# Performance work log

Hardware: AMD Instinct MI355X
Metric: run time of the kernel (lower is better)

Reference implementation:

```python
import jax, jax.numpy as jnp
import numpy as np

B, S, R, H = 32, 512, 49, 768


def setup_inputs() -> dict:
    key = jax.random.key(0)
    ks = jax.random.split(key, 32)
    rn = lambda i, shape, s=1.0: jax.random.normal(ks[i], shape, dtype=jnp.float32) * s
    W = 0.05  # weight init scale to keep tanh/softmax in a sane range
    return {
        'text_features': rn(0, (B, S, H)),
        'img_features': rn(1, (B, R, H)),
        't1_w': rn(2, (H, H), W), 't1_b': rn(3, (H,), W),
        'i1_w': rn(4, (H, H), W),
        'a1_w': rn(5, (2 * H,), W), 'a1_b': rn(6, (), W),
        't2_w': rn(7, (H, H), W),
        'i2_w': rn(8, (H, H), W), 'i2_b': rn(9, (H,), W),
        'a2_w': rn(10, (2 * H,), W), 'a2_b': rn(11, (), W),
        'gt_w': rn(12, (H, H), W), 'gt_b': rn(13, (H,), W),
        'gi_w': rn(14, (H, H), W), 'gi_b': rn(15, (H,), W),
        'gg_w': rn(16, (2 * H, 1), W), 'gg_b': rn(17, (1,), W),
        'ft_w': rn(18, (H, H), W),
        'fm_w': rn(19, (H, H), W), 'fm_b': rn(20, (H,), W),
        'fg_w': rn(21, (2 * H, 1), W), 'fg_b': rn(22, (1,), W),
        'fr_w': rn(23, (H, H), W), 'fr_b': rn(24, (H,), W),
    }


def reference(text_features, img_features, t1_w, t1_b, i1_w, a1_w, a1_b,
              t2_w, i2_w, i2_b, a2_w, a2_b, gt_w, gt_b, gi_w, gi_b,
              gg_w, gg_b, ft_w, fm_w, fm_b, fg_w, fg_b, fr_w, fr_b):
    H = text_features.shape[-1]
    # --- CoAttention, stage 1 (text attends over image regions) ---
    # tanh(concat) is elementwise and att_linear_1 is rank-1, so split the score:
    # score[b,s,r] = tanh(t1(x_s)) . a1[:H] + tanh(i1(y_r)) . a1[H:] + b
    t_sc = jnp.tanh(text_features @ t1_w + t1_b) @ a1_w[:H]          # (B,S)
    i_sc = jnp.tanh(img_features @ i1_w) @ a1_w[H:]                  # (B,R)
    visual_att = jax.nn.softmax(t_sc[:, :, None] + i_sc[:, None, :] + a1_b, axis=-1)  # (B,S,R)
    att_img = jnp.einsum('bsr,brh->bsh', visual_att, img_features)   # (B,S,H)
    # --- CoAttention, stage 2 (attended-image queries attend over text) ---
    # concat order is [img, text] -> a2[:H] pairs with img part
    q_sc = jnp.tanh(att_img @ i2_w + i2_b) @ a2_w[:H]                # (B,S)
    k_sc = jnp.tanh(text_features @ t2_w) @ a2_w[H:]                 # (B,S)
    textual_att = jax.nn.softmax(q_sc[:, :, None] + k_sc[:, None, :] + a2_b, axis=-1)  # (B,S,S)
    att_text = jnp.einsum('bij,bjh->bih', textual_att, text_features)  # (B,S,H)
    # --- GMF gated fusion ---
    new_img = jnp.tanh(att_img @ gi_w + gi_b)
    new_txt = jnp.tanh(att_text @ gt_w + gt_b)
    gate = jax.nn.sigmoid(jnp.concatenate([new_img, new_txt], axis=-1) @ gg_w + gg_b)  # (B,S,1)
    multimodal = gate * new_img + (1.0 - gate) * new_txt
    # --- filtration gate ---
    concat_feat = jnp.concatenate([text_features @ ft_w, multimodal @ fm_w + fm_b], axis=-1)
    fgate = jax.nn.sigmoid(concat_feat @ fg_w + fg_b)                # (B,S,1)
    return fgate * jnp.tanh(multimodal @ fr_w + fr_b)
```

## Files before the change

### kernel.cpp

```cpp
#include <hip/hip_runtime.h>
#include <hip/hip_bf16.h>
#include <math.h>

constexpr int BD = 32;
constexpr int SD = 512;
constexpr int RD = 49;
constexpr int HD = 768;
constexpr int NB = HD / 64;
constexpr int NP = NB * 2;
constexpr int MT = BD * SD;
constexpr int MI = BD * RD;

typedef __bf16 bf16;
typedef __bf16 bf16x4 __attribute__((ext_vector_type(4)));
typedef __bf16 bf16x8 __attribute__((ext_vector_type(8)));
typedef float f32x4 __attribute__((ext_vector_type(4)));

__global__ __launch_bounds__(256) void prep_text(
    const float* __restrict__ text, const float* __restrict__ v_f,
    bf16* __restrict__ text_bf, float* __restrict__ s_txt)
{
    const int row = blockIdx.x * 4 + (threadIdx.x >> 6);
    const int lane = threadIdx.x & 63;
    const float* tr = text + (size_t)row * HD;
    bf16* tb = text_bf + (size_t)row * HD;
    float acc = 0.f;
    #pragma unroll
    for (int c = 0; c < 3; ++c) {
        const int o = c * 256 + lane * 4;
        const f32x4 x = *(const f32x4*)(tr + o);
        const f32x4 v = *(const f32x4*)(v_f + o);
        bf16x4 b; b[0] = (bf16)x[0]; b[1] = (bf16)x[1]; b[2] = (bf16)x[2]; b[3] = (bf16)x[3];
        *(bf16x4*)(tb + o) = b;
        acc += x[0] * v[0] + x[1] * v[1] + x[2] * v[2] + x[3] * v[3];
    }
    for (int off = 32; off; off >>= 1) acc += __shfl_xor(acc, off);
    if (lane == 0) s_txt[row] = acc;
}

__global__ __launch_bounds__(256) void conv_img(const float* __restrict__ src,
                                                bf16* __restrict__ dst, int n8) {
    const int i = blockIdx.x * 256 + threadIdx.x;
    if (i >= n8) return;
    const size_t o = (size_t)i * 8;
    const f32x4 x0 = *(const f32x4*)(src + o);
    const f32x4 x1 = *(const f32x4*)(src + o + 4);
    bf16x8 b;
    b[0]=(bf16)x0[0]; b[1]=(bf16)x0[1]; b[2]=(bf16)x0[2]; b[3]=(bf16)x0[3];
    b[4]=(bf16)x1[0]; b[5]=(bf16)x1[1]; b[6]=(bf16)x1[2]; b[7]=(bf16)x1[3];
    *(bf16x8*)(dst + o) = b;
}

__global__ __launch_bounds__(256) void transpose_w(
    const float* __restrict__ w0, const float* __restrict__ w1,
    bf16* __restrict__ o0, bf16* __restrict__ o1)
{
    __shared__ float tile[64][65];
    const float* W = blockIdx.z ? w1 : w0;
    bf16* Wt = blockIdx.z ? o1 : o0;
    const int k0 = blockIdx.x * 64, n0 = blockIdx.y * 64;
    const int t = threadIdx.x;
    const int rb = t >> 6, c = t & 63;
    #pragma unroll
    for (int i = 0; i < 16; ++i) {
        const int r = rb + i * 4;
        tile[r][c] = W[(size_t)(k0 + r) * HD + n0 + c];
    }
    __syncthreads();
    #pragma unroll
    for (int i = 0; i < 16; ++i) {
        const int r = rb + i * 4;
        Wt[(size_t)(n0 + r) * HD + k0 + c] = (bf16)tile[c][r];
    }
}

__global__ __launch_bounds__(256) void gemm_bt(
    const bf16* __restrict__ A, const bf16* __restrict__ Wt,
    const float* __restrict__ vec, float* __restrict__ part, int M)
{
    __shared__ __align__(16) bf16 As[64][40];
    __shared__ __align__(16) bf16 Bs[64][40];

    const int t = threadIdx.x;
    const int m0 = blockIdx.x * 64;
    const int n0 = blockIdx.y * 64;
    const int w = t >> 6, lane = t & 63;
    const int quad = lane >> 4, l16 = lane & 15;
    const int wm = (w >> 1) * 32, wn = (w & 1) * 32;

    const int r = t >> 2, c8 = (t & 3) * 8;
    const int gm = m0 + r;
    const bf16* Ap = A + (size_t)gm * HD + c8;
    const bf16* Bp = Wt + (size_t)(n0 + r) * HD + c8;

    f32x4 acc[2][2] = {};

    for (int kk = 0; kk < HD; kk += 32) {
        bf16x8 av = {};
        if (gm < M) av = *(const bf16x8*)(Ap + kk);
        const bf16x8 bv = *(const bf16x8*)(Bp + kk);

        __syncthreads();
        *(bf16x8*)(&As[r][c8]) = av;
        *(bf16x8*)(&Bs[r][c8]) = bv;
        __syncthreads();

        const bf16x8 a0 = *(const bf16x8*)(&As[wm + l16][quad * 8]);
        const bf16x8 a1 = *(const bf16x8*)(&As[wm + 16 + l16][quad * 8]);
        const bf16x8 b0 = *(const bf16x8*)(&Bs[wn + l16][quad * 8]);
        const bf16x8 b1 = *(const bf16x8*)(&Bs[wn + 16 + l16][quad * 8]);
        acc[0][0] = __builtin_amdgcn_mfma_f32_16x16x32_bf16(a0, b0, acc[0][0], 0, 0, 0);
        acc[0][1] = __builtin_amdgcn_mfma_f32_16x16x32_bf16(a0, b1, acc[0][1], 0, 0, 0);
        acc[1][0] = __builtin_amdgcn_mfma_f32_16x16x32_bf16(a1, b0, acc[1][0], 0, 0, 0);
        acc[1][1] = __builtin_amdgcn_mfma_f32_16x16x32_bf16(a1, b1, acc[1][1], 0, 0, 0);
    }

    #pragma unroll
    for (int ti = 0; ti < 2; ++ti)
      #pragma unroll
      for (int reg = 0; reg < 4; ++reg) {
          float p = 0.f;
          #pragma unroll
          for (int tj = 0; tj < 2; ++tj) {
              const int gn = n0 + wn + tj * 16 + l16;
              p += tanhf(acc[ti][tj][reg]) * vec[gn];
          }
          p += __shfl_xor(p, 1);
          p += __shfl_xor(p, 2);
          p += __shfl_xor(p, 4);
          p += __shfl_xor(p, 8);
          const int gm2 = m0 + wm + ti * 16 + quad * 4 + reg;
          if (l16 == 0) part[(size_t)gm2 * NP + blockIdx.y * 2 + (w & 1)] = p;
      }
}

__global__ __launch_bounds__(256) void reduce_nb(const float* __restrict__ part,
                                                 float* __restrict__ score, int M) {
    const int m = blockIdx.x * 256 + threadIdx.x;
    if (m < M) {
        float s = 0.f;
        #pragma unroll
        for (int j = 0; j < NP; ++j) s += part[(size_t)m * NP + j];
        score[m] = s;
    }
}

__global__ __launch_bounds__(64) void softmax_p1(const float* sc, float* p1) {
    const int b = blockIdx.x, l = threadIdx.x;
    float x = (l < RD) ? sc[b * RD + l] : -1e30f;
    float m = x;
    for (int off = 32; off; off >>= 1) m = fmaxf(m, __shfl_xor(m, off));
    float e = (l < RD) ? expf(x - m) : 0.f;
    float s = e;
    for (int off = 32; off; off >>= 1) s += __shfl_xor(s, off);
    if (l < RD) p1[b * RD + l] = e / s;
}

__global__ __launch_bounds__(256) void softmax_p2(const float* sc, float* p2) {
    const int b = blockIdx.x, t = threadIdx.x;
    __shared__ float red[4];
    const float x0 = sc[b * SD + t], x1 = sc[b * SD + 256 + t];
    float m = fmaxf(x0, x1);
    for (int off = 32; off; off >>= 1) m = fmaxf(m, __shfl_xor(m, off));
    if ((t & 63) == 0) red[t >> 6] = m;
    __syncthreads();
    m = fmaxf(fmaxf(red[0], red[1]), fmaxf(red[2], red[3]));
    const float e0 = expf(x0 - m), e1 = expf(x1 - m);
    float s = e0 + e1;
    for (int off = 32; off; off >>= 1) s += __shfl_xor(s, off);
    __syncthreads();
    if ((t & 63) == 0) red[t >> 6] = s;
    __syncthreads();
    s = red[0] + red[1] + red[2] + red[3];
    p2[b * SD + t] = e0 / s;
    p2[b * SD + 256 + t] = e1 / s;
}

__global__ __launch_bounds__(256) void wsum_rows(const float* __restrict__ P,
                                                 const float* __restrict__ X,
                                                 float* __restrict__ Y, int J) {
    const int b = blockIdx.x;
    const int h = blockIdx.y * 256 + threadIdx.x;
    __shared__ float Ps[SD];
    for (int j = threadIdx.x; j < J; j += 256) Ps[j] = P[b * J + j];
    __syncthreads();
    float acc = 0.f;
    const float* Xb = X + (size_t)b * J * HD + h;
    for (int j = 0; j < J; ++j) acc += Ps[j] * Xb[(size_t)j * HD];
    Y[b * HD + h] = acc;
}

__global__ __launch_bounds__(256) void wsum_part(const float* __restrict__ P,
                                                 const bf16* __restrict__ X,
                                                 float* __restrict__ part) {
    const int b = blockIdx.x;
    const int h = blockIdx.y * 256 + threadIdx.x;
    const int q = blockIdx.z;
    __shared__ float Ps[128];
    if (threadIdx.x < 128) Ps[threadIdx.x] = P[b * SD + q * 128 + threadIdx.x];
    __syncthreads();
    float acc = 0.f;
    const bf16* Xb = X + (size_t)b * SD * HD + (size_t)(q * 128) * HD + h;
    #pragma unroll 8
    for (int j = 0; j < 128; ++j) acc += Ps[j] * (float)Xb[(size_t)j * HD];
    part[((size_t)(b * 4 + q)) * HD + h] = acc;
}

__global__ __launch_bounds__(256) void wsum_reduce(const float* __restrict__ part,
                                                   float* __restrict__ Y) {
    const int m = blockIdx.x * 256 + threadIdx.x;
    const int b = m / HD, h = m % HD;
    float s = 0.f;
    #pragma unroll
    for (int q = 0; q < 4; ++q) s += part[((size_t)(b * 4 + q)) * HD + h];
    Y[m] = s;
}

__global__ __launch_bounds__(256) void ni_nt_kernel(
    const float* __restrict__ aimg, const float* __restrict__ atxt,
    const float* __restrict__ gi_w, const float* __restrict__ gi_b,
    const float* __restrict__ gt_w, const float* __restrict__ gt_b,
    float* __restrict__ ni, float* __restrict__ nt)
{
    const int b = blockIdx.x, n0 = blockIdx.y * 64, which = blockIdx.z;
    const float* X = which ? atxt : aimg;
    const float* W = which ? gt_w : gi_w;
    const float* bias = which ? gt_b : gi_b;
    float* Y = which ? nt : ni;

    __shared__ float Xs[HD];
    __shared__ float partial[4][64];
    const int t = threadIdx.x;
    for (int h = t; h < HD; h += 256) Xs[h] = X[b * HD + h];
    __syncthreads();
    const int n = n0 + (t & 63), kq = t >> 6;
    float acc = 0.f;
    const float* Wp = W + (size_t)(kq * 192) * HD + n;
    #pragma unroll 8
    for (int h = 0; h < 192; ++h) acc += Xs[kq * 192 + h] * Wp[(size_t)h * HD];
    partial[kq][t & 63] = acc;
    __syncthreads();
    if (t < 64) {
        const float s = partial[0][t] + partial[1][t] + partial[2][t] + partial[3][t];
        Y[b * HD + n0 + t] = tanhf(s + bias[n0 + t]);
    }
}

__global__ __launch_bounds__(256) void gate_mix(
    const float* __restrict__ ni, const float* __restrict__ nt,
    const float* __restrict__ gg_w, const float* __restrict__ gg_b,
    const float* __restrict__ v_m, const float* __restrict__ c_m,
    const float* __restrict__ fg_b,
    float* __restrict__ mm, float* __restrict__ s_mm)
{
    const int b = blockIdx.x, t = threadIdx.x;
    __shared__ float red[4];
    __shared__ float gsh;
    float acc = 0.f;
    for (int n = t; n < HD; n += 256)
        acc += ni[b * HD + n] * gg_w[n] + nt[b * HD + n] * gg_w[HD + n];
    for (int off = 32; off; off >>= 1) acc += __shfl_xor(acc, off);
    if ((t & 63) == 0) red[t >> 6] = acc;
    __syncthreads();
    if (t == 0) gsh = 1.f / (1.f + expf(-(red[0] + red[1] + red[2] + red[3] + gg_b[0])));
    __syncthreads();
    const float g = gsh;
    float a2 = 0.f;
    for (int n = t; n < HD; n += 256) {
        const float m = g * ni[b * HD + n] + (1.f - g) * nt[b * HD + n];
        mm[b * HD + n] = m;
        a2 += m * v_m[n];
    }
    for (int off = 32; off; off >>= 1) a2 += __shfl_xor(a2, off);
    __syncthreads();
    if ((t & 63) == 0) red[t >> 6] = a2;
    __syncthreads();
    if (t == 0) s_mm[b] = red[0] + red[1] + red[2] + red[3] + *c_m + fg_b[0];
}

__global__ __launch_bounds__(256) void T_kernel(
    const float* __restrict__ mm, const float* __restrict__ fr_w,
    const float* __restrict__ fr_b, float* __restrict__ T)
{
    const int b = blockIdx.x, n0 = blockIdx.y * 64;
    __shared__ float Xs[HD];
    __shared__ float partial[4][64];
    const int t = threadIdx.x;
    for (int h = t; h < HD; h += 256) Xs[h] = mm[b * HD + h];
    __syncthreads();
    const int n = n0 + (t & 63), kq = t >> 6;
    float acc = 0.f;
    const float* Wp = fr_w + (size_t)(kq * 192) * HD + n;
    #pragma unroll 8
    for (int h = 0; h < 192; ++h) acc += Xs[kq * 192 + h] * Wp[(size_t)h * HD];
    partial[kq][t & 63] = acc;
    __syncthreads();
    if (t < 64) {
        const float s = partial[0][t] + partial[1][t] + partial[2][t] + partial[3][t];
        T[b * HD + n0 + t] = tanhf(s + fr_b[n0 + t]);
    }
}

__global__ __launch_bounds__(256) void vf_vm_kernel(const float* __restrict__ ft_w,
                                                    const float* __restrict__ fm_w,
                                                    const float* __restrict__ fm_b,
                                                    const float* __restrict__ fg_w,
                                                    float* __restrict__ v_f,
                                                    float* __restrict__ v_m,
                                                    float* __restrict__ c_m) {
    const int idx = blockIdx.x * 4 + (threadIdx.x >> 6);
    const int lane = threadIdx.x & 63;
    const float* row; const float* vecp; float* outp;
    if (idx < HD)            { row = ft_w + (size_t)idx * HD;        vecp = fg_w;      outp = v_f + idx; }
    else if (idx < 2 * HD)   { row = fm_w + (size_t)(idx - HD) * HD; vecp = fg_w + HD; outp = v_m + (idx - HD); }
    else if (idx == 2 * HD)  { row = fm_b;                           vecp = fg_w + HD; outp = c_m; }
    else return;
    float acc = 0.f;
    #pragma unroll
    for (int i = 0; i < HD / 64; ++i) acc += row[lane + 64 * i] * vecp[lane + 64 * i];
    for (int off = 32; off; off >>= 1) acc += __shfl_xor(acc, off);
    if (lane == 0) *outp = acc;
}

__global__ __launch_bounds__(256) void out_kernel(const float* __restrict__ s_txt,
                                                  const float* __restrict__ s_mm,
                                                  const float* __restrict__ T,
                                                  float* __restrict__ out) {
    const size_t idx = ((size_t)blockIdx.x * 256 + threadIdx.x) * 4;
    const int h = (int)(idx % HD);
    const int bs = (int)(idx / HD);
    const int b = bs >> 9;
    float f = s_txt[bs] + s_mm[b];
    f = 1.f / (1.f + expf(-f));
    const float* Tp = T + b * HD + h;
    f32x4 o;
    o[0] = f * Tp[0]; o[1] = f * Tp[1]; o[2] = f * Tp[2]; o[3] = f * Tp[3];
    *(f32x4*)(out + idx) = o;
}

extern "C" void kernel_launch(void* const* d_in, const int* in_sizes, int n_in,
                              void* d_out, int out_size, void* d_ws, size_t ws_size,
                              hipStream_t stream) {
    const float* text = (const float*)d_in[0];
    const float* img  = (const float*)d_in[1];
    const float* i1_w = (const float*)d_in[4];
    const float* a1_w = (const float*)d_in[5];
    const float* t2_w = (const float*)d_in[7];
    const float* a2_w = (const float*)d_in[10];
    const float* gt_w = (const float*)d_in[12];
    const float* gt_b = (const float*)d_in[13];
    const float* gi_w = (const float*)d_in[14];
    const float* gi_b = (const float*)d_in[15];
    const float* gg_w = (const float*)d_in[16];
    const float* gg_b = (const float*)d_in[17];
    const float* ft_w = (const float*)d_in[18];
    const float* fm_w = (const float*)d_in[19];
    const float* fm_b = (const float*)d_in[20];
    const float* fg_w = (const float*)d_in[21];
    const float* fg_b = (const float*)d_in[22];
    const float* fr_w = (const float*)d_in[23];
    const float* fr_b = (const float*)d_in[24];
    float* out = (float*)d_out;

    float* sc_ = out;
    float* i_part  = sc_;
    float* k_part  = sc_ + 38400;
    float* i_sc    = sc_ + 431616;
    float* k_sc    = sc_ + 433216;
    float* aimg    = sc_ + 449600;
    float* atxt    = sc_ + 474176;
    float* v_f     = sc_ + 498752;
    float* v_m     = sc_ + 499520;
    float* c_m     = sc_ + 500288;
    float* ws_part = sc_ + 500352;
    float* ni      = sc_ + 598656;
    float* nt      = sc_ + 623232;
    float* mm      = sc_ + 647808;
    bf16* text_bf  = (bf16*)(sc_ + 672384);
    bf16* img_bf   = (bf16*)(sc_ + 6963840);
    bf16* wt_t     = (bf16*)(sc_ + 7565952);
    bf16* wt_i     = (bf16*)(sc_ + 7860864);

    float* ws    = (float*)d_ws;
    float* s_txt = ws;
    float* s_mm  = ws + 16384;
    float* T     = ws + 16448;

    vf_vm_kernel<<<dim3((2 * HD + 1 + 3) / 4), dim3(256), 0, stream>>>(
        ft_w, fm_w, fm_b, fg_w, v_f, v_m, c_m);
    prep_text<<<dim3(MT / 4), dim3(256), 0, stream>>>(text, v_f, text_bf, s_txt);
    conv_img<<<dim3((BD * RD * HD / 8 + 255) / 256), dim3(256), 0, stream>>>(
        img, img_bf, BD * RD * HD / 8);
    transpose_w<<<dim3(12, 12, 2), dim3(256), 0, stream>>>(t2_w, i1_w, wt_t, wt_i);
    gemm_bt<<<dim3((MI + 63) / 64, NB), dim3(256), 0, stream>>>(
        img_bf, wt_i, a1_w + HD, i_part, MI);
    gemm_bt<<<dim3(MT / 64, NB), dim3(256), 0, stream>>>(
        text_bf, wt_t, a2_w + HD, k_part, MT);
    reduce_nb<<<dim3(7), dim3(256), 0, stream>>>(i_part, i_sc, MI);
    reduce_nb<<<dim3(MT / 256), dim3(256), 0, stream>>>(k_part, k_sc, MT);
    softmax_p1<<<dim3(BD), dim3(64), 0, stream>>>(i_sc, i_sc);
    softmax_p2<<<dim3(BD), dim3(256), 0, stream>>>(k_sc, k_sc);
    wsum_rows<<<dim3(BD, HD / 256), dim3(256), 0, stream>>>(i_sc, img, aimg, RD);
    wsum_part<<<dim3(BD, HD / 256, 4), dim3(256), 0, stream>>>(k_sc, text_bf, ws_part);
    wsum_reduce<<<dim3(BD * HD / 256), dim3(256), 0, stream>>>(ws_part, atxt);
    ni_nt_kernel<<<dim3(BD, HD / 64, 2), dim3(256), 0, stream>>>(
        aimg, atxt, gi_w, gi_b, gt_w, gt_b, ni, nt);
    gate_mix<<<dim3(BD), dim3(256), 0, stream>>>(
        ni, nt, gg_w, gg_b, v_m, c_m, fg_b, mm, s_mm);
    T_kernel<<<dim3(BD, HD / 64), dim3(256), 0, stream>>>(mm, fr_w, fr_b, T);
    out_kernel<<<dim3((MT * HD / 4) / 256), dim3(256), 0, stream>>>(s_txt, s_mm, T, out);
}
```

Measured before the change: 293.9 us.

## Retile score GEMM with direct-to-LDS loads and merge small kernels

Replaces the two 64x64 score GEMMs with one combined launch. It uses 128x128 tiles, a 4x4 MFMA fragment grid per wave and global_load_lds to copy tiles straight into shared memory, and swaps tanhf for an exp-based fast tanh in the epilogue. It also merges weight prep, image conversion and transpose, the two reductions, the two softmaxes and the two weighted sums into single launches. The text weighted-sum reduction moves into the gating kernel. The goal is more data reuse in the dominant GEMM and fewer kernel launches, at the cost of unpadded LDS tiles that may bank-conflict and padded image rows that read past the image buffer into neighbouring scratch.

```diff
diff --git a/kernel.cpp b/kernel.cpp
--- a/kernel.cpp
+++ b/kernel.cpp
@@ -6,15 +6,25 @@
 constexpr int SD = 512;
 constexpr int RD = 49;
 constexpr int HD = 768;
-constexpr int NB = HD / 64;
-constexpr int NP = NB * 2;
 constexpr int MT = BD * SD;
 constexpr int MI = BD * RD;
+constexpr int NP = 12;
+constexpr int MBT = MT / 128;
+constexpr int MBI = 13;
 
 typedef __bf16 bf16;
 typedef __bf16 bf16x4 __attribute__((ext_vector_type(4)));
 typedef __bf16 bf16x8 __attribute__((ext_vector_type(8)));
 typedef float f32x4 __attribute__((ext_vector_type(4)));
+
+#define GLOAD_LDS16(g, l) __builtin_amdgcn_global_load_lds( \
+    (__attribute__((address_space(1))) void*)(g),           \
+    (__attribute__((address_space(3))) void*)(l), 16, 0, 0)
+
+__device__ __forceinline__ float fast_tanh(float x) {
+    const float e = __expf(2.f * x);
+    return 1.f - 2.f / (e + 1.f);
+}
 
 __global__ __launch_bounds__(256) void prep_text(
     const float* __restrict__ text, const float* __restrict__ v_f,
@@ -38,192 +48,234 @@
     if (lane == 0) s_txt[row] = acc;
 }
 
-__global__ __launch_bounds__(256) void conv_img(const float* __restrict__ src,
-                                                bf16* __restrict__ dst, int n8) {
-    const int i = blockIdx.x * 256 + threadIdx.x;
-    if (i >= n8) return;
-    const size_t o = (size_t)i * 8;
-    const f32x4 x0 = *(const f32x4*)(src + o);
-    const f32x4 x1 = *(const f32x4*)(src + o + 4);
-    bf16x8 b;
-    b[0]=(bf16)x0[0]; b[1]=(bf16)x0[1]; b[2]=(bf16)x0[2]; b[3]=(bf16)x0[3];
-    b[4]=(bf16)x1[0]; b[5]=(bf16)x1[1]; b[6]=(bf16)x1[2]; b[7]=(bf16)x1[3];
-    *(bf16x8*)(dst + o) = b;
-}
-
-__global__ __launch_bounds__(256) void transpose_w(
-    const float* __restrict__ w0, const float* __restrict__ w1,
-    bf16* __restrict__ o0, bf16* __restrict__ o1)
+__global__ __launch_bounds__(256) void prep_misc(
+    const float* __restrict__ ft_w, const float* __restrict__ fm_w,
+    const float* __restrict__ fm_b, const float* __restrict__ fg_w,
+    float* __restrict__ v_f, float* __restrict__ v_m, float* __restrict__ c_m,
+    const float* __restrict__ img, bf16* __restrict__ img_bf,
+    const float* __restrict__ t2_w, const float* __restrict__ i1_w,
+    bf16* __restrict__ wt_t, bf16* __restrict__ wt_i)
 {
     __shared__ float tile[64][65];
-    const float* W = blockIdx.z ? w1 : w0;
-    bf16* Wt = blockIdx.z ? o1 : o0;
-    const int k0 = blockIdx.x * 64, n0 = blockIdx.y * 64;
+    const int bid = blockIdx.x;
+    if (bid < 385) {
+        const int idx = bid * 4 + (threadIdx.x >> 6);
+        const int lane = threadIdx.x & 63;
+        const float* row; const float* vecp; float* outp;
+        if (idx < HD)            { row = ft_w + (size_t)idx * HD;        vecp = fg_w;      outp = v_f + idx; }
+        else if (idx < 2 * HD)   { row = fm_w + (size_t)(idx - HD) * HD; vecp = fg_w + HD; outp = v_m + (idx - HD); }
+        else if (idx == 2 * HD)  { row = fm_b;                           vecp = fg_w + HD; outp = c_m; }
+        else return;
+        float acc = 0.f;
+        #pragma unroll
+        for (int i = 0; i < HD / 64; ++i) acc += row[lane + 64 * i] * vecp[lane + 64 * i];
+        for (int off = 32; off; off >>= 1) acc += __shfl_xor(acc, off);
+        if (lane == 0) *outp = acc;
+    } else if (bid < 385 + 588) {
+        const int i = (bid - 385) * 256 + threadIdx.x;
+        const int n8 = BD * RD * HD / 8;
+        if (i >= n8) return;
+        const size_t o = (size_t)i * 8;
+        const f32x4 x0 = *(const f32x4*)(img + o);
+        const f32x4 x1 = *(const f32x4*)(img + o + 4);
+        bf16x8 b;
+        b[0]=(bf16)x0[0]; b[1]=(bf16)x0[1]; b[2]=(bf16)x0[2]; b[3]=(bf16)x0[3];
+        b[4]=(bf16)x1[0]; b[5]=(bf16)x1[1]; b[6]=(bf16)x1[2]; b[7]=(bf16)x1[3];
+        *(bf16x8*)(img_bf + o) = b;
+    } else {
+        const int idx2 = bid - (385 + 588);
+        const int z = idx2 / 144, rem = idx2 % 144;
+        const int bx = rem % 12, by = rem / 12;
+        const float* W = z ? i1_w : t2_w;
+        bf16* Wt = z ? wt_i : wt_t;
+        const int k0 = bx * 64, n0 = by * 64;
+        const int t = threadIdx.x;
+        const int rb = t >> 6, c = t & 63;
+        #pragma unroll
+        for (int i = 0; i < 16; ++i) {
+            const int r = rb + i * 4;
+            tile[r][c] = W[(size_t)(k0 + r) * HD + n0 + c];
+        }
+        __syncthreads();
+        #pragma unroll
+        for (int i = 0; i < 16; ++i) {
+            const int r = rb + i * 4;
+            Wt[(size_t)(n0 + r) * HD + k0 + c] = (bf16)tile[c][r];
+        }
+    }
+}
+
+__global__ __launch_bounds__(256) void gemm2(
+    const bf16* __restrict__ Atext, const bf16* __restrict__ WtT,
+    const float* __restrict__ vecT, float* __restrict__ partT,
+    const bf16* __restrict__ Aimg, const bf16* __restrict__ WtI,
+    const float* __restrict__ vecI, float* __restrict__ partI)
+{
+    __shared__ __align__(16) bf16 As[128 * 32];
+    __shared__ __align__(16) bf16 Bs[128 * 32];
+
+    const bool isT = blockIdx.x < MBT;
+    const bf16* A   = isT ? Atext : Aimg;
+    const bf16* Wt  = isT ? WtT : WtI;
+    const float* vec = isT ? vecT : vecI;
+    float* part     = isT ? partT : partI;
+    const int m0 = (isT ? blockIdx.x : blockIdx.x - MBT) * 128;
+    const int n0 = blockIdx.y * 128;
+
     const int t = threadIdx.x;
-    const int rb = t >> 6, c = t & 63;
-    #pragma unroll
-    for (int i = 0; i < 16; ++i) {
-        const int r = rb + i * 4;
-        tile[r][c] = W[(size_t)(k0 + r) * HD + n0 + c];
-    }
-    __syncthreads();
-    #pragma unroll
-    for (int i = 0; i < 16; ++i) {
-        const int r = rb + i * 4;
-        Wt[(size_t)(n0 + r) * HD + k0 + c] = (bf16)tile[c][r];
-    }
-}
-
-__global__ __launch_bounds__(256) void gemm_bt(
-    const bf16* __restrict__ A, const bf16* __restrict__ Wt,
-    const float* __restrict__ vec, float* __restrict__ part, int M)
-{
-    __shared__ __align__(16) bf16 As[64][40];
-    __shared__ __align__(16) bf16 Bs[64][40];
-
-    const int t = threadIdx.x;
-    const int m0 = blockIdx.x * 64;
-    const int n0 = blockIdx.y * 64;
     const int w = t >> 6, lane = t & 63;
     const int quad = lane >> 4, l16 = lane & 15;
-    const int wm = (w >> 1) * 32, wn = (w & 1) * 32;
-
-    const int r = t >> 2, c8 = (t & 3) * 8;
-    const int gm = m0 + r;
-    const bf16* Ap = A + (size_t)gm * HD + c8;
-    const bf16* Bp = Wt + (size_t)(n0 + r) * HD + c8;
-
-    f32x4 acc[2][2] = {};
+    const int wm2 = (w >> 1) * 64, wn2 = (w & 1) * 64;
+
+    const int srow = lane >> 2;
+    const int scol = (lane & 3) * 8;
+    const bf16* Ag = A  + (size_t)(m0 + w * 32 + srow) * HD + scol;
+    const bf16* Bg = Wt + (size_t)(n0 + w * 32 + srow) * HD + scol;
+    bf16* Al0 = As + (w * 32) * 32;
+    bf16* Al1 = As + (w * 32 + 16) * 32;
+    bf16* Bl0 = Bs + (w * 32) * 32;
+    bf16* Bl1 = Bs + (w * 32 + 16) * 32;
+
+    f32x4 acc[4][4] = {};
 
     for (int kk = 0; kk < HD; kk += 32) {
-        bf16x8 av = {};
-        if (gm < M) av = *(const bf16x8*)(Ap + kk);
-        const bf16x8 bv = *(const bf16x8*)(Bp + kk);
-
-        __syncthreads();
-        *(bf16x8*)(&As[r][c8]) = av;
-        *(bf16x8*)(&Bs[r][c8]) = bv;
-        __syncthreads();
-
-        const bf16x8 a0 = *(const bf16x8*)(&As[wm + l16][quad * 8]);
-        const bf16x8 a1 = *(const bf16x8*)(&As[wm + 16 + l16][quad * 8]);
-        const bf16x8 b0 = *(const bf16x8*)(&Bs[wn + l16][quad * 8]);
-        const bf16x8 b1 = *(const bf16x8*)(&Bs[wn + 16 + l16][quad * 8]);
-        acc[0][0] = __builtin_amdgcn_mfma_f32_16x16x32_bf16(a0, b0, acc[0][0], 0, 0, 0);
-        acc[0][1] = __builtin_amdgcn_mfma_f32_16x16x32_bf16(a0, b1, acc[0][1], 0, 0, 0);
-        acc[1][0] = __builtin_amdgcn_mfma_f32_16x16x32_bf16(a1, b0, acc[1][0], 0, 0, 0);
-        acc[1][1] = __builtin_amdgcn_mfma_f32_16x16x32_bf16(a1, b1, acc[1][1], 0, 0, 0);
-    }
-
+        GLOAD_LDS16(Ag + kk, Al0);
+        GLOAD_LDS16(Ag + (size_t)16 * HD + kk, Al1);
+        GLOAD_LDS16(Bg + kk, Bl0);
+        GLOAD_LDS16(Bg + (size_t)16 * HD + kk, Bl1);
+        __syncthreads();
+
+        bf16x8 af[4], bg[4];
+        #pragma unroll
+        for (int f = 0; f < 4; ++f) {
+            af[f] = *(const bf16x8*)(&As[(wm2 + f * 16 + l16) * 32 + quad * 8]);
+            bg[f] = *(const bf16x8*)(&Bs[(wn2 + f * 16 + l16) * 32 + quad * 8]);
+        }
+        #pragma unroll
+        for (int fi = 0; fi < 4; ++fi)
+            #pragma unroll
+            for (int fj = 0; fj < 4; ++fj)
+                acc[fi][fj] = __builtin_amdgcn_mfma_f32_16x16x32_bf16(af[fi], bg[fj], acc[fi][fj], 0, 0, 0);
+        __syncthreads();
+    }
+
+    float vv[4];
     #pragma unroll
-    for (int ti = 0; ti < 2; ++ti)
-      #pragma unroll
-      for (int reg = 0; reg < 4; ++reg) {
-          float p = 0.f;
-          #pragma unroll
-          for (int tj = 0; tj < 2; ++tj) {
-              const int gn = n0 + wn + tj * 16 + l16;
-              p += tanhf(acc[ti][tj][reg]) * vec[gn];
-          }
-          p += __shfl_xor(p, 1);
-          p += __shfl_xor(p, 2);
-          p += __shfl_xor(p, 4);
-          p += __shfl_xor(p, 8);
-          const int gm2 = m0 + wm + ti * 16 + quad * 4 + reg;
-          if (l16 == 0) part[(size_t)gm2 * NP + blockIdx.y * 2 + (w & 1)] = p;
-      }
-}
-
-__global__ __launch_bounds__(256) void reduce_nb(const float* __restrict__ part,
-                                                 float* __restrict__ score, int M) {
+    for (int fj = 0; fj < 4; ++fj) vv[fj] = vec[n0 + wn2 + fj * 16 + l16];
+
+    #pragma unroll
+    for (int fi = 0; fi < 4; ++fi) {
+        #pragma unroll
+        for (int reg = 0; reg < 4; ++reg) {
+            float p = 0.f;
+            #pragma unroll
+            for (int fj = 0; fj < 4; ++fj)
+                p += fast_tanh(acc[fi][fj][reg]) * vv[fj];
+            p += __shfl_xor(p, 1);
+            p += __shfl_xor(p, 2);
+            p += __shfl_xor(p, 4);
+            p += __shfl_xor(p, 8);
+            if (l16 == 0) {
+                const int row = m0 + wm2 + fi * 16 + quad * 4 + reg;
+                part[(size_t)row * NP + blockIdx.y * 2 + (w & 1)] = p;
+            }
+        }
+    }
+}
+
+__global__ __launch_bounds__(256) void reduce2(
+    const float* __restrict__ k_part, const float* __restrict__ i_part,
+    float* __restrict__ k_sc, float* __restrict__ i_sc)
+{
     const int m = blockIdx.x * 256 + threadIdx.x;
-    if (m < M) {
+    if (m < MT) {
         float s = 0.f;
         #pragma unroll
-        for (int j = 0; j < NP; ++j) s += part[(size_t)m * NP + j];
-        score[m] = s;
-    }
-}
-
-__global__ __launch_bounds__(64) void softmax_p1(const float* sc, float* p1) {
-    const int b = blockIdx.x, l = threadIdx.x;
-    float x = (l < RD) ? sc[b * RD + l] : -1e30f;
-    float m = x;
-    for (int off = 32; off; off >>= 1) m = fmaxf(m, __shfl_xor(m, off));
-    float e = (l < RD) ? expf(x - m) : 0.f;
-    float s = e;
-    for (int off = 32; off; off >>= 1) s += __shfl_xor(s, off);
-    if (l < RD) p1[b * RD + l] = e / s;
-}
-
-__global__ __launch_bounds__(256) void softmax_p2(const float* sc, float* p2) {
-    const int b = blockIdx.x, t = threadIdx.x;
+        for (int j = 0; j < NP; ++j) s += k_part[(size_t)m * NP + j];
+        k_sc[m] = s;
+    } else {
+        const int m2 = m - MT;
+        if (m2 < MI) {
+            float s = 0.f;
+            #pragma unroll
+            for (int j = 0; j < NP; ++j) s += i_part[(size_t)m2 * NP + j];
+            i_sc[m2] = s;
+        }
+    }
+}
+
+__global__ __launch_bounds__(256) void softmax_both(float* k_sc, float* i_sc) {
     __shared__ float red[4];
-    const float x0 = sc[b * SD + t], x1 = sc[b * SD + 256 + t];
-    float m = fmaxf(x0, x1);
-    for (int off = 32; off; off >>= 1) m = fmaxf(m, __shfl_xor(m, off));
-    if ((t & 63) == 0) red[t >> 6] = m;
-    __syncthreads();
-    m = fmaxf(fmaxf(red[0], red[1]), fmaxf(red[2], red[3]));
-    const float e0 = expf(x0 - m), e1 = expf(x1 - m);
-    float s = e0 + e1;
-    for (int off = 32; off; off >>= 1) s += __shfl_xor(s, off);
-    __syncthreads();
-    if ((t & 63) == 0) red[t >> 6] = s;
-    __syncthreads();
-    s = red[0] + red[1] + red[2] + red[3];
-    p2[b * SD + t] = e0 / s;
-    p2[b * SD + 256 + t] = e1 / s;
-}
-
-__global__ __launch_bounds__(256) void wsum_rows(const float* __restrict__ P,
-                                                 const float* __restrict__ X,
-                                                 float* __restrict__ Y, int J) {
-    const int b = blockIdx.x;
-    const int h = blockIdx.y * 256 + threadIdx.x;
+    if (blockIdx.x < BD) {
+        const int b = blockIdx.x, t = threadIdx.x;
+        const float x0 = k_sc[b * SD + t], x1 = k_sc[b * SD + 256 + t];
+        float m = fmaxf(x0, x1);
+        for (int off = 32; off; off >>= 1) m = fmaxf(m, __shfl_xor(m, off));
+        if ((t & 63) == 0) red[t >> 6] = m;
+        __syncthreads();
+        m = fmaxf(fmaxf(red[0], red[1]), fmaxf(red[2], red[3]));
+        const float e0 = expf(x0 - m), e1 = expf(x1 - m);
+        float s = e0 + e1;
+        for (int off = 32; off; off >>= 1) s += __shfl_xor(s, off);
+        __syncthreads();
+        if ((t & 63) == 0) red[t >> 6] = s;
+        __syncthreads();
+        s = red[0] + red[1] + red[2] + red[3];
+        k_sc[b * SD + t] = e0 / s;
+        k_sc[b * SD + 256 + t] = e1 / s;
+    } else {
+        const int b = blockIdx.x - BD, l = threadIdx.x;
+        if (l < 64) {
+            float x = (l < RD) ? i_sc[b * RD + l] : -1e30f;
+            float m = x;
+            for (int off = 32; off; off >>= 1) m = fmaxf(m, __shfl_xor(m, off));
+            float e = (l < RD) ? expf(x - m) : 0.f;
+            float s = e;
+            for (int off = 32; off; off >>= 1) s += __shfl_xor(s, off);
+            if (l < RD) i_sc[b * RD + l] = e / s;
+        }
+    }
+}
+
+__global__ __launch_bounds__(256) void wsum_both(
+    const float* __restrict__ P1, const float* __restrict__ img,
+    float* __restrict__ aimg,
+    const float* __restrict__ P2, const bf16* __restrict__ text_bf,
+    float* __restrict__ ws_part)
+{
     __shared__ float Ps[SD];
-    for (int j = threadIdx.x; j < J; j += 256) Ps[j] = P[b * J + j];
-    __syncthreads();
-    float acc = 0.f;
-    const float* Xb = X + (size_t)b * J * HD + h;
-    for (int j = 0; j < J; ++j) acc += Ps[j] * Xb[(size_t)j * HD];
-    Y[b * HD + h] = acc;
-}
-
-__global__ __launch_bounds__(256) void wsum_part(const float* __restrict__ P,
-                                                 const bf16* __restrict__ X,
-                                                 float* __restrict__ part) {
-    const int b = blockIdx.x;
-    const int h = blockIdx.y * 256 + threadIdx.x;
-    const int q = blockIdx.z;
-    __shared__ float Ps[128];
-    if (threadIdx.x < 128) Ps[threadIdx.x] = P[b * SD + q * 128 + threadIdx.x];
-    __syncthreads();
-    float acc = 0.f;
-    const bf16* Xb = X + (size_t)b * SD * HD + (size_t)(q * 128) * HD + h;
-    #pragma unroll 8
-    for (int j = 0; j < 128; ++j) acc += Ps[j] * (float)Xb[(size_t)j * HD];
-    part[((size_t)(b * 4 + q)) * HD + h] = acc;
-}
-
-__global__ __launch_bounds__(256) void wsum_reduce(const float* __restrict__ part,
-                                                   float* __restrict__ Y) {
-    const int m = blockIdx.x * 256 + threadIdx.x;
-    const int b = m / HD, h = m % HD;
-    float s = 0.f;
-    #pragma unroll
-    for (int q = 0; q < 4; ++q) s += part[((size_t)(b * 4 + q)) * HD + h];
-    Y[m] = s;
+    const int bid = blockIdx.x;
+    if (bid < 96) {
+        const int b = bid & 31, hy = bid >> 5;
+        const int h = hy * 256 + threadIdx.x;
+        for (int j = threadIdx.x; j < RD; j += 256) Ps[j] = P1[b * RD + j];
+        __syncthreads();
+        float acc = 0.f;
+        const float* Xb = img + (size_t)b * RD * HD + h;
+        for (int j = 0; j < RD; ++j) acc += Ps[j] * Xb[(size_t)j * HD];
+        aimg[b * HD + h] = acc;
+    } else {
+        const int idx = bid - 96;
+        const int q = idx / 96, rem = idx % 96;
+        const int b = rem & 31, hy = rem >> 5;
+        const int h = hy * 256 + threadIdx.x;
+        if (threadIdx.x < 128) Ps[threadIdx.x] = P2[b * SD + q * 128 + threadIdx.x];
+        __syncthreads();
+        float acc = 0.f;
+        const bf16* Xb = text_bf + (size_t)b * SD * HD + (size_t)(q * 128) * HD + h;
+        #pragma unroll 8
+        for (int j = 0; j < 128; ++j) acc += Ps[j] * (float)Xb[(size_t)j * HD];
+        ws_part[((size_t)(b * 4 + q)) * HD + h] = acc;
+    }
 }
 
 __global__ __launch_bounds__(256) void ni_nt_kernel(
-    const float* __restrict__ aimg, const float* __restrict__ atxt,
+    const float* __restrict__ aimg, const float* __restrict__ ws_part,
     const float* __restrict__ gi_w, const float* __restrict__ gi_b,
     const float* __restrict__ gt_w, const float* __restrict__ gt_b,
     float* __restrict__ ni, float* __restrict__ nt)
 {
     const int b = blockIdx.x, n0 = blockIdx.y * 64, which = blockIdx.z;
-    const float* X = which ? atxt : aimg;
     const float* W = which ? gt_w : gi_w;
     const float* bias = which ? gt_b : gi_b;
     float* Y = which ? nt : ni;
@@ -231,7 +283,13 @@
     __shared__ float Xs[HD];
     __shared__ float partial[4][64];
     const int t = threadIdx.x;
-    for (int h = t; h < HD; h += 256) Xs[h] = X[b * HD + h];
+    if (which) {
+        for (int h = t; h < HD; h += 256)
+            Xs[h] = ws_part[((size_t)(b * 4 + 0)) * HD + h] + ws_part[((size_t)(b * 4 + 1)) * HD + h]
+                  + ws_part[((size_t)(b * 4 + 2)) * HD + h] + ws_part[((size_t)(b * 4 + 3)) * HD + h];
+    } else {
+        for (int h = t; h < HD; h += 256) Xs[h] = aimg[b * HD + h];
+    }
     __syncthreads();
     const int n = n0 + (t & 63), kq = t >> 6;
     float acc = 0.f;
@@ -299,27 +357,6 @@
         const float s = partial[0][t] + partial[1][t] + partial[2][t] + partial[3][t];
         T[b * HD + n0 + t] = tanhf(s + fr_b[n0 + t]);
     }
-}
-
-__global__ __launch_bounds__(256) void vf_vm_kernel(const float* __restrict__ ft_w,
-                                                    const float* __restrict__ fm_w,
-                                                    const float* __restrict__ fm_b,
-                                                    const float* __restrict__ fg_w,
-                                                    float* __restrict__ v_f,
-                                                    float* __restrict__ v_m,
-                                                    float* __restrict__ c_m) {
-    const int idx = blockIdx.x * 4 + (threadIdx.x >> 6);
-    const int lane = threadIdx.x & 63;
-    const float* row; const float* vecp; float* outp;
-    if (idx < HD)            { row = ft_w + (size_t)idx * HD;        vecp = fg_w;      outp = v_f + idx; }
-    else if (idx < 2 * HD)   { row = fm_w + (size_t)(idx - HD) * HD; vecp = fg_w + HD; outp = v_m + (idx - HD); }
-    else if (idx == 2 * HD)  { row = fm_b;                           vecp = fg_w + HD; outp = c_m; }
-    else return;
-    float acc = 0.f;
-    #pragma unroll
-    for (int i = 0; i < HD / 64; ++i) acc += row[lane + 64 * i] * vecp[lane + 64 * i];
-    for (int off = 32; off; off >>= 1) acc += __shfl_xor(acc, off);
-    if (lane == 0) *outp = acc;
 }
 
 __global__ __launch_bounds__(256) void out_kernel(const float* __restrict__ s_txt,
@@ -368,7 +405,6 @@
     float* i_sc    = sc_ + 431616;
     float* k_sc    = sc_ + 433216;
     float* aimg    = sc_ + 449600;
-    float* atxt    = sc_ + 474176;
     float* v_f     = sc_ + 498752;
     float* v_m     = sc_ + 499520;
     float* c_m     = sc_ + 500288;
@@ -386,25 +422,18 @@
     float* s_mm  = ws + 16384;
     float* T     = ws + 16448;
 
-    vf_vm_kernel<<<dim3((2 * HD + 1 + 3) / 4), dim3(256), 0, stream>>>(
-        ft_w, fm_w, fm_b, fg_w, v_f, v_m, c_m);
+    prep_misc<<<dim3(385 + 588 + 288), dim3(256), 0, stream>>>(
+        ft_w, fm_w, fm_b, fg_w, v_f, v_m, c_m, img, img_bf, t2_w, i1_w, wt_t, wt_i);
     prep_text<<<dim3(MT / 4), dim3(256), 0, stream>>>(text, v_f, text_bf, s_txt);
-    conv_img<<<dim3((BD * RD * HD / 8 + 255) / 256), dim3(256), 0, stream>>>(
-        img, img_bf, BD * RD * HD / 8);
-    transpose_w<<<dim3(12, 12, 2), dim3(256), 0, stream>>>(t2_w, i1_w, wt_t, wt_i);
-    gemm_bt<<<dim3((MI + 63) / 64, NB), dim3(256), 0, stream>>>(
-        img_bf, wt_i, a1_w + HD, i_part, MI);
-    gemm_bt<<<dim3(MT / 64, NB), dim3(256), 0, stream>>>(
-        text_bf, wt_t, a2_w + HD, k_part, MT);
-    reduce_nb<<<dim3(7), dim3(256), 0, stream>>>(i_part, i_sc, MI);
-    reduce_nb<<<dim3(MT / 256), dim3(256), 0, stream>>>(k_part, k_sc, MT);
-    softmax_p1<<<dim3(BD), dim3(64), 0, stream>>>(i_sc, i_sc);
-    softmax_p2<<<dim3(BD), dim3(256), 0, stream>>>(k_sc, k_sc);
-    wsum_rows<<<dim3(BD, HD / 256), dim3(256), 0, stream>>>(i_sc, img, aimg, RD);
-    wsum_part<<<dim3(BD, HD / 256, 4), dim3(256), 0, stream>>>(k_sc, text_bf, ws_part);
-    wsum_reduce<<<dim3(BD * HD / 256), dim3(256), 0, stream>>>(ws_part, atxt);
+    gemm2<<<dim3(MBT + MBI, 6), dim3(256), 0, stream>>>(
+        text_bf, wt_t, a2_w + HD, k_part, img_bf, wt_i, a1_w + HD, i_part);
+    reduce2<<<dim3(MT / 256 + (MI + 255) / 256), dim3(256), 0, stream>>>(
+        k_part, i_part, k_sc, i_sc);
+    softmax_both<<<dim3(2 * BD), dim3(256), 0, stream>>>(k_sc, i_sc);
+    wsum_both<<<dim3(96 + 384), dim3(256), 0, stream>>>(
+        i_sc, img, aimg, k_sc, text_bf, ws_part);
     ni_nt_kernel<<<dim3(BD, HD / 64, 2), dim3(256), 0, stream>>>(
-        aimg, atxt, gi_w, gi_b, gt_w, gt_b, ni, nt);
+        aimg, ws_part, gi_w, gi_b, gt_w, gt_b, ni, nt);
     gate_mix<<<dim3(BD), dim3(256), 0, stream>>>(
         ni, nt, gg_w, gg_b, v_m, c_m, fg_b, mm, s_mm);
     T_kernel<<<dim3(BD, HD / 64), dim3(256), 0, stream>>>(mm, fr_w, fr_b, T);
```

Measured after the change: 267.1 us. 9.1% less time.
